# Optimization experiments

Hardware: AMD Instinct MI355X
Metric: run time of the kernel (lower is better)

Reference implementation:

```python
import jax, jax.numpy as jnp
import numpy as np

HEAD_DIM = 64

def setup_inputs() -> dict:
    key = jax.random.key(0)
    kq, kk, kv = jax.random.split(key, 3)
    shape = (2, 4096, 8, HEAD_DIM)  # [B, S, H, D]
    q = jax.random.normal(kq, shape, dtype=jnp.float32)
    k = jax.random.normal(kk, shape, dtype=jnp.float32)
    v = jax.random.normal(kv, shape, dtype=jnp.float32)
    return {"q": q, "k": k, "v": v}

def reference(q, k, v):
    # Single-process path of SimpleRingAttention: standard softmax attention.
    # q,k,v: [B, S, H, D]; scores computed per head.
    scale = 1.0 / jnp.sqrt(jnp.asarray(HEAD_DIM, dtype=q.dtype))
    scores = jnp.einsum('bqhd,bkhd->bhqk', q, k) * scale  # [B,H,S,S]
    attn = jax.nn.softmax(scores, axis=-1)
    out = jnp.einsum('bhqk,bkhd->bqhd', attn, v)  # back to [B,S,H,D]
    return out
```

## Files before the change

kernel.cpp:

```cpp
#include <hip/hip_runtime.h>
#include <hip/hip_bf16.h>

#define B_ 2
#define S_ 4096
#define H_ 8
#define D_ 64
#define BQ 128
#define BK 64

#define GLOBAL_AS __attribute__((address_space(1)))
#define LDS_AS    __attribute__((address_space(3)))

typedef short bf16x8 __attribute__((ext_vector_type(8)));
typedef short bf16x4 __attribute__((ext_vector_type(4)));
typedef float f32x4  __attribute__((ext_vector_type(4)));
typedef float f32x16 __attribute__((ext_vector_type(16)));
typedef unsigned int u32x4 __attribute__((ext_vector_type(4)));

#define QSCALE 0.18033688011112043f

__device__ __forceinline__ short f2bf(float f) {
    __bf16 h = (__bf16)f;
    return __builtin_bit_cast(short, h);
}

__device__ __forceinline__ bf16x8 pack8(float4 f0, float4 f1) {
    bf16x8 r;
    r[0]=f2bf(f0.x); r[1]=f2bf(f0.y); r[2]=f2bf(f0.z); r[3]=f2bf(f0.w);
    r[4]=f2bf(f1.x); r[5]=f2bf(f1.y); r[6]=f2bf(f1.z); r[7]=f2bf(f1.w);
    return r;
}

__device__ __forceinline__ bf16x8 pack8s(float4 f0, float4 f1, float s) {
    bf16x8 r;
    r[0]=f2bf(f0.x*s); r[1]=f2bf(f0.y*s); r[2]=f2bf(f0.z*s); r[3]=f2bf(f0.w*s);
    r[4]=f2bf(f1.x*s); r[5]=f2bf(f1.y*s); r[6]=f2bf(f1.z*s); r[7]=f2bf(f1.w*s);
    return r;
}

__device__ __forceinline__ unsigned pkbf(float a, float b) {
    unsigned ua = (unsigned)(unsigned short)__builtin_bit_cast(unsigned short, (__bf16)a);
    unsigned ub = (unsigned)(unsigned short)__builtin_bit_cast(unsigned short, (__bf16)b);
    return ua | (ub << 16);
}

__device__ __forceinline__ void perm32swap(unsigned &a, unsigned &b) {
    asm("v_permlane32_swap_b32 %0, %1" : "+v"(a), "+v"(b));
}

__global__ __launch_bounds__(256) void cast_kv_kernel(
    const float* __restrict__ kin, const float* __restrict__ vin,
    unsigned short* __restrict__ kb, unsigned short* __restrict__ vtb)
{
    __shared__ float Lf[64][72];
    const int role = blockIdx.z & 1;
    const int b    = blockIdx.z >> 1;
    const int h    = blockIdx.y;
    const int s0   = blockIdx.x * 64;
    const int t    = threadIdx.x;

    if (role == 0) {
        int r = t >> 2, fq = t & 3;
        const float4* gp = (const float4*)(kin + (((size_t)(b*S_ + s0 + r)*H_ + h)*D_ + fq*16));
        bf16x8 o0 = pack8(gp[0], gp[1]);
        bf16x8 o1 = pack8(gp[2], gp[3]);
        unsigned short* ob = kb + ((size_t)(b*H_ + h)*S_ + s0 + r)*D_ + fq*16;
        *(bf16x8*)ob       = o0;
        *(bf16x8*)(ob + 8) = o1;
    } else {
        {
            int r  = t >> 2, fq = t & 3;
            const float4* gp = (const float4*)(vin + (((size_t)(b*S_ + s0 + r)*H_ + h)*D_ + fq*16));
            #pragma unroll
            for (int j = 0; j < 4; ++j)
                *(f32x4*)&Lf[r][fq*16 + 4*j] = (f32x4){gp[j].x, gp[j].y, gp[j].z, gp[j].w};
        }
        __syncthreads();
        {
            int d = t >> 2, sq = t & 3;
            bf16x8 o0, o1;
            #pragma unroll
            for (int j = 0; j < 8; ++j) o0[j] = f2bf(Lf[sq*16 + j][d]);
            #pragma unroll
            for (int j = 0; j < 8; ++j) o1[j] = f2bf(Lf[sq*16 + 8 + j][d]);
            unsigned short* ob = vtb + (((size_t)(b*H_ + h)*D_ + d)*S_ + s0 + sq*16);
            *(bf16x8*)(ob)     = o0;
            *(bf16x8*)(ob + 8) = o1;
        }
    }
}

template<bool SPLIT>
__global__ __launch_bounds__(256, 4) void fattn_kernel(
    const float* __restrict__ q, const unsigned short* __restrict__ kb,
    const unsigned short* __restrict__ vtb, float* __restrict__ out,
    float* __restrict__ Op, float* __restrict__ lw)
{
    __shared__ unsigned short Ks [BK][64];
    __shared__ unsigned short Vts[D_][64];

    const int tid  = threadIdx.x;
    const int wave = tid >> 6;
    const int lane = tid & 63;
    const int l31  = tid & 31;
    const int hi   = lane >> 5;
    const int h    = blockIdx.y;
    const int b    = SPLIT ? (blockIdx.z >> 1) : blockIdx.z;
    const int half = SPLIT ? (blockIdx.z & 1)  : 0;
    const int kt0  = half * 32;
    const int nkt  = SPLIT ? 32 : 64;
    const int q0   = blockIdx.x * BQ;
    const int bS   = b * S_;
    const int wq   = wave * 32;

    int aoff[2][4];
    #pragma unroll
    for (int t = 0; t < 2; ++t)
        #pragma unroll
        for (int kc = 0; kc < 4; ++kc)
            aoff[t][kc] = (t*32 + l31)*64 + (((kc*2 + hi) ^ (l31 & 7))*8);

    const int srow = (lane >> 3);
    const int c8g  = (lane & 7) ^ srow;
    const int wqs  = wave * 16;
    const unsigned short* ksg[2];
    const unsigned short* vtg[2];
    #pragma unroll
    for (int it = 0; it < 2; ++it) {
        int rk = wqs + it*8 + srow;
        ksg[it] = kb  + ((size_t)(b*H_ + h)*S_ + rk)*64 + c8g*8;
        vtg[it] = vtb + ((size_t)(b*H_ + h)*D_ + rk)*(size_t)S_ + c8g*8;
    }

    bf16x8 bq[4];
    {
        const int qrow = q0 + wq + l31;
        const float* qp = q + ((size_t)(bS + qrow)*H_ + h)*D_;
        #pragma unroll
        for (int kc = 0; kc < 4; ++kc) {
            const float4* q4 = (const float4*)(qp + kc*16 + hi*8);
            bq[kc] = pack8s(q4[0], q4[1], QSCALE);
        }
    }

    f32x16 oacc[2];
    #pragma unroll
    for (int dt = 0; dt < 2; ++dt)
        #pragma unroll
        for (int r = 0; r < 16; ++r) oacc[dt][r] = 0.f;
    float lp0 = 0.f, lp1 = 0.f;

    for (int i = 0; i < nkt; ++i) {
        const int kt = kt0 + i;
        __syncthreads();
        #pragma unroll
        for (int it = 0; it < 2; ++it) {
            __builtin_amdgcn_global_load_lds(
                (const GLOBAL_AS void*)(ksg[it] + (size_t)kt*BK*64),
                (LDS_AS void*)&Ks[wqs + it*8][0], 16, 0, 0);
            __builtin_amdgcn_global_load_lds(
                (const GLOBAL_AS void*)(vtg[it] + (size_t)kt*BK),
                (LDS_AS void*)&Vts[wqs + it*8][0], 16, 0, 0);
        }
        __syncthreads();

        #pragma unroll
        for (int mt = 0; mt < 2; ++mt) {
            f32x16 s;
            #pragma unroll
            for (int r = 0; r < 16; ++r) s[r] = 0.f;
            #pragma unroll
            for (int kc = 0; kc < 4; ++kc) {
                bf16x8 aK = *(const bf16x8*)&Ks[0][aoff[mt][kc]];
                s = __builtin_amdgcn_mfma_f32_32x32x16_bf16(aK, bq[kc], s, 0,0,0);
            }

            unsigned pk_[8];
            #pragma unroll
            for (int r = 0; r < 8; ++r) {
                float e0 = __builtin_exp2f(s[2*r]);
                float e1 = __builtin_exp2f(s[2*r+1]);
                lp0 += e0; lp1 += e1;
                pk_[r] = pkbf(e0, e1);
            }
            perm32swap(pk_[0], pk_[2]);
            perm32swap(pk_[1], pk_[3]);
            perm32swap(pk_[4], pk_[6]);
            perm32swap(pk_[5], pk_[7]);
            u32x4 w0 = {pk_[0], pk_[1], pk_[2], pk_[3]};
            u32x4 w1 = {pk_[4], pk_[5], pk_[6], pk_[7]};
            bf16x8 bp0 = __builtin_bit_cast(bf16x8, w0);
            bf16x8 bp1 = __builtin_bit_cast(bf16x8, w1);

            #pragma unroll
            for (int dt = 0; dt < 2; ++dt) {
                bf16x8 aV0 = *(const bf16x8*)&Vts[0][aoff[dt][mt*2 + 0]];
                oacc[dt] = __builtin_amdgcn_mfma_f32_32x32x16_bf16(aV0, bp0, oacc[dt], 0,0,0);
                bf16x8 aV1 = *(const bf16x8*)&Vts[0][aoff[dt][mt*2 + 1]];
                oacc[dt] = __builtin_amdgcn_mfma_f32_32x32x16_bf16(aV1, bp1, oacc[dt], 0,0,0);
            }
        }
    }

    float lt0 = lp0 + lp1;
    float lt  = lt0 + __shfl_xor(lt0, 32);
    const int orow = q0 + wq + l31;
    if constexpr (SPLIT) {
        float* ob = Op + (size_t)half*((size_t)B_*S_*H_*D_)
                       + ((size_t)(bS + orow)*H_ + h)*D_;
        #pragma unroll
        for (int dt = 0; dt < 2; ++dt)
            #pragma unroll
            for (int rg = 0; rg < 4; ++rg) {
                float4 o4 = { oacc[dt][rg*4+0], oacc[dt][rg*4+1],
                              oacc[dt][rg*4+2], oacc[dt][rg*4+3] };
                *(float4*)(ob + dt*32 + rg*8 + hi*4) = o4;
            }
        if (hi == 0)
            lw[(size_t)half*((size_t)B_*S_*H_) + (size_t)(bS + orow)*H_ + h] = lt;
    } else {
        const float linv = 1.0f / lt;
        float* ob = out + ((size_t)(bS + orow)*H_ + h)*D_;
        #pragma unroll
        for (int dt = 0; dt < 2; ++dt)
            #pragma unroll
            for (int rg = 0; rg < 4; ++rg) {
                float4 o4 = { oacc[dt][rg*4+0]*linv, oacc[dt][rg*4+1]*linv,
                              oacc[dt][rg*4+2]*linv, oacc[dt][rg*4+3]*linv };
                *(float4*)(ob + dt*32 + rg*8 + hi*4) = o4;
            }
    }
}

__global__ __launch_bounds__(256) void combine_kernel(
    const float* __restrict__ Op, const float* __restrict__ lw,
    float* __restrict__ out)
{
    const size_t NR = (size_t)B_*S_*H_;
    const size_t NO = NR * D_;
    const int t = threadIdx.x;
    size_t r  = (size_t)blockIdx.x * 16 + (t >> 4);
    int   c4  = t & 15;
    const float4* p0 = (const float4*)(Op + r*D_) + c4;
    const float4* p1 = (const float4*)(Op + NO + r*D_) + c4;
    float linv = 1.0f / (lw[r] + lw[NR + r]);
    float4 a = *p0, b = *p1;
    float4 o = { (a.x+b.x)*linv, (a.y+b.y)*linv, (a.z+b.z)*linv, (a.w+b.w)*linv };
    *((float4*)(out + r*D_) + c4) = o;
}

#define FBQ 64
#define LDK 72
__global__ __launch_bounds__(256, 4) void fattn_fb(
    const float* __restrict__ q, const float* __restrict__ k,
    const float* __restrict__ v, float* __restrict__ out)
{
    __shared__ unsigned short Ks [BK][LDK];
    __shared__ unsigned short Vts[D_][LDK];
    __shared__ unsigned short Ps [FBQ][LDK];
    const int tid  = threadIdx.x;
    const int wave = tid >> 6;
    const int m16  = tid & 15;
    const int quad = (tid & 63) >> 4;
    const int h    = blockIdx.y;
    const int b    = blockIdx.z;
    const int q0   = blockIdx.x * FBQ;
    const int bS   = b * S_;
    const int wq   = wave * 16;
    bf16x8 bq[2];
    {
        const int qrow = q0 + wq + m16;
        const float* qb = q + ((size_t)(bS + qrow)*H_ + h)*D_;
        #pragma unroll
        for (int kh = 0; kh < 2; ++kh) {
            const float4* qp = (const float4*)(qb + kh*32 + quad*8);
            bq[kh] = pack8s(qp[0], qp[1], QSCALE);
        }
    }
    const short ONE = 0x3F80;
    bf16x8 ones = { ONE,ONE,ONE,ONE,ONE,ONE,ONE,ONE };
    f32x4 oacc[4];
    f32x4 lacc = (f32x4){0.f,0.f,0.f,0.f};
    #pragma unroll
    for (int dt = 0; dt < 4; ++dt) oacc[dt] = (f32x4){0.f,0.f,0.f,0.f};
    const int vd  = tid & 63;
    const int vkg = tid >> 6;
    for (int kt = 0; kt < S_/BK; ++kt) {
        const int k0 = kt * BK;
        __syncthreads();
        #pragma unroll
        for (int i = 0; i < 2; ++i) {
            int chunk = tid + i*256;
            int row = chunk >> 3, c8 = chunk & 7;
            const float4* gp = (const float4*)(k + ((size_t)(bS + k0 + row)*H_ + h)*D_ + c8*8);
            *(bf16x8*)&Ks[row][c8*8] = pack8(gp[0], gp[1]);
        }
        {
            const float* vb = v + ((size_t)(bS + k0 + vkg*16)*H_ + h)*D_ + vd;
            bf16x8 t0, t1;
            #pragma unroll
            for (int i = 0; i < 8; ++i) t0[i] = f2bf(vb[(size_t)i * (H_*D_)]);
            #pragma unroll
            for (int i = 0; i < 8; ++i) t1[i] = f2bf(vb[(size_t)(i+8) * (H_*D_)]);
            *(bf16x8*)&Vts[vd][vkg*16]     = t0;
            *(bf16x8*)&Vts[vd][vkg*16 + 8] = t1;
        }
        __syncthreads();
        f32x4 sacc[4];
        #pragma unroll
        for (int mt = 0; mt < 4; ++mt) sacc[mt] = (f32x4){0.f,0.f,0.f,0.f};
        #pragma unroll
        for (int kh = 0; kh < 2; ++kh)
            #pragma unroll
            for (int mt = 0; mt < 4; ++mt) {
                bf16x8 aK = *(const bf16x8*)&Ks[mt*16 + m16][kh*32 + quad*8];
                sacc[mt] = __builtin_amdgcn_mfma_f32_16x16x32_bf16(aK, bq[kh], sacc[mt], 0,0,0);
            }
        #pragma unroll
        for (int mt = 0; mt < 4; ++mt) {
            bf16x4 pk;
            #pragma unroll
            for (int r = 0; r < 4; ++r)
                pk[r] = f2bf(__builtin_exp2f(sacc[mt][r]));
            *(bf16x4*)&Ps[wq + m16][mt*16 + quad*4] = pk;
        }
        #pragma unroll
        for (int kh = 0; kh < 2; ++kh) {
            bf16x8 bp = *(const bf16x8*)&Ps[wq + m16][kh*32 + quad*8];
            lacc = __builtin_amdgcn_mfma_f32_16x16x32_bf16(ones, bp, lacc, 0,0,0);
            #pragma unroll
            for (int dt = 0; dt < 4; ++dt) {
                bf16x8 aV = *(const bf16x8*)&Vts[dt*16 + m16][kh*32 + quad*8];
                oacc[dt] = __builtin_amdgcn_mfma_f32_16x16x32_bf16(aV, bp, oacc[dt], 0,0,0);
            }
        }
    }
    const float linv = 1.0f / lacc[0];
    const int orow = q0 + wq + m16;
    float* ob = out + ((size_t)(bS + orow)*H_ + h)*D_;
    #pragma unroll
    for (int dt = 0; dt < 4; ++dt) {
        float4 o4 = { oacc[dt][0]*linv, oacc[dt][1]*linv,
                      oacc[dt][2]*linv, oacc[dt][3]*linv };
        *(float4*)(ob + dt*16 + quad*4) = o4;
    }
}

extern "C" void kernel_launch(void* const* d_in, const int* in_sizes, int n_in,
                              void* d_out, int out_size, void* d_ws, size_t ws_size,
                              hipStream_t stream) {
    const float* q = (const float*)d_in[0];
    const float* k = (const float*)d_in[1];
    const float* v = (const float*)d_in[2];
    float* out = (float*)d_out;
    const size_t elems = (size_t)B_*H_*S_*D_;
    const size_t NR    = (size_t)B_*S_*H_;
    const size_t need_cast  = 2 * elems * sizeof(unsigned short);
    const size_t need_split = need_cast + 2*elems*sizeof(float) + 2*NR*sizeof(float);

    if (ws_size >= need_split) {
        unsigned short* kb  = (unsigned short*)d_ws;
        unsigned short* vtb = kb + elems;
        float* Op = (float*)(vtb + elems);
        float* lw = Op + 2*elems;
        cast_kv_kernel<<<dim3(S_/64, H_, B_*2), dim3(256), 0, stream>>>(k, v, kb, vtb);
        fattn_kernel<true><<<dim3(S_/BQ, H_, B_*2), dim3(256), 0, stream>>>(
            q, kb, vtb, out, Op, lw);
        combine_kernel<<<dim3((int)(NR/16)), dim3(256), 0, stream>>>(Op, lw, out);
    } else if (ws_size >= need_cast) {
        unsigned short* kb  = (unsigned short*)d_ws;
        unsigned short* vtb = kb + elems;
        cast_kv_kernel<<<dim3(S_/64, H_, B_*2), dim3(256), 0, stream>>>(k, v, kb, vtb);
        fattn_kernel<false><<<dim3(S_/BQ, H_, B_), dim3(256), 0, stream>>>(
            q, kb, vtb, out, nullptr, nullptr);
    } else {
        fattn_fb<<<dim3(S_/FBQ, H_, B_), dim3(256), 0, stream>>>(q, k, v, out);
    }
}
```

Before: 209.3 us.

## Double-buffer K/V tiles in LDS with async prefetch of next tile

Adds a second LDS buffer for K and V tiles and issues the global-to-LDS loads for tile i+1 before computing tile i. Manual vmcnt waits and raw s_barrier replace the two __syncthreads per iteration, and s_setprio raises wave priority around the MFMA section. The goal is to hide global load latency behind the matrix work. In exchange it doubles LDS use per block, which may reduce occupancy, and it depends on the hand-written waitcnt counts being correct.

```diff
diff --git a/kernel.cpp b/kernel.cpp
--- a/kernel.cpp
+++ b/kernel.cpp
@@ -96,8 +96,8 @@
     const unsigned short* __restrict__ vtb, float* __restrict__ out,
     float* __restrict__ Op, float* __restrict__ lw)
 {
-    __shared__ unsigned short Ks [BK][64];
-    __shared__ unsigned short Vts[D_][64];
+    __shared__ unsigned short Ks [2][BK][64];
+    __shared__ unsigned short Vts[2][D_][64];
 
     const int tid  = threadIdx.x;
     const int wave = tid >> 6;
@@ -150,20 +150,38 @@
         for (int r = 0; r < 16; ++r) oacc[dt][r] = 0.f;
     float lp0 = 0.f, lp1 = 0.f;
 
+    #pragma unroll
+    for (int it = 0; it < 2; ++it) {
+        __builtin_amdgcn_global_load_lds(
+            (const GLOBAL_AS void*)(ksg[it] + (size_t)kt0*BK*64),
+            (LDS_AS void*)&Ks[0][wqs + it*8][0], 16, 0, 0);
+        __builtin_amdgcn_global_load_lds(
+            (const GLOBAL_AS void*)(vtg[it] + (size_t)kt0*BK),
+            (LDS_AS void*)&Vts[0][wqs + it*8][0], 16, 0, 0);
+    }
+
     for (int i = 0; i < nkt; ++i) {
-        const int kt = kt0 + i;
-        __syncthreads();
-        #pragma unroll
-        for (int it = 0; it < 2; ++it) {
-            __builtin_amdgcn_global_load_lds(
-                (const GLOBAL_AS void*)(ksg[it] + (size_t)kt*BK*64),
-                (LDS_AS void*)&Ks[wqs + it*8][0], 16, 0, 0);
-            __builtin_amdgcn_global_load_lds(
-                (const GLOBAL_AS void*)(vtg[it] + (size_t)kt*BK),
-                (LDS_AS void*)&Vts[wqs + it*8][0], 16, 0, 0);
-        }
-        __syncthreads();
-
+        const int cur = i & 1;
+        if (i + 1 < nkt) {
+            const int kt = kt0 + i + 1;
+            #pragma unroll
+            for (int it = 0; it < 2; ++it) {
+                __builtin_amdgcn_global_load_lds(
+                    (const GLOBAL_AS void*)(ksg[it] + (size_t)kt*BK*64),
+                    (LDS_AS void*)&Ks[cur ^ 1][wqs + it*8][0], 16, 0, 0);
+                __builtin_amdgcn_global_load_lds(
+                    (const GLOBAL_AS void*)(vtg[it] + (size_t)kt*BK),
+                    (LDS_AS void*)&Vts[cur ^ 1][wqs + it*8][0], 16, 0, 0);
+            }
+            asm volatile("s_waitcnt vmcnt(4)" ::: "memory");
+        } else {
+            asm volatile("s_waitcnt vmcnt(0)" ::: "memory");
+        }
+        __builtin_amdgcn_sched_barrier(0);
+        __builtin_amdgcn_s_barrier();
+        __builtin_amdgcn_sched_barrier(0);
+
+        __builtin_amdgcn_s_setprio(1);
         #pragma unroll
         for (int mt = 0; mt < 2; ++mt) {
             f32x16 s;
@@ -171,7 +189,7 @@
             for (int r = 0; r < 16; ++r) s[r] = 0.f;
             #pragma unroll
             for (int kc = 0; kc < 4; ++kc) {
-                bf16x8 aK = *(const bf16x8*)&Ks[0][aoff[mt][kc]];
+                bf16x8 aK = *(const bf16x8*)&Ks[cur][0][aoff[mt][kc]];
                 s = __builtin_amdgcn_mfma_f32_32x32x16_bf16(aK, bq[kc], s, 0,0,0);
             }
 
@@ -194,12 +212,15 @@
 
             #pragma unroll
             for (int dt = 0; dt < 2; ++dt) {
-                bf16x8 aV0 = *(const bf16x8*)&Vts[0][aoff[dt][mt*2 + 0]];
+                bf16x8 aV0 = *(const bf16x8*)&Vts[cur][0][aoff[dt][mt*2 + 0]];
                 oacc[dt] = __builtin_amdgcn_mfma_f32_32x32x16_bf16(aV0, bp0, oacc[dt], 0,0,0);
-                bf16x8 aV1 = *(const bf16x8*)&Vts[0][aoff[dt][mt*2 + 1]];
+                bf16x8 aV1 = *(const bf16x8*)&Vts[cur][0][aoff[dt][mt*2 + 1]];
                 oacc[dt] = __builtin_amdgcn_mfma_f32_32x32x16_bf16(aV1, bp1, oacc[dt], 0,0,0);
             }
         }
+        __builtin_amdgcn_s_setprio(0);
+        __builtin_amdgcn_sched_barrier(0);
+        __builtin_amdgcn_s_barrier();
     }
 
     float lt0 = lp0 + lp1;
```

Result: no change. 206.0 us (-1.6%).

## Split each key tile across two wave groups and reduce partial outputs in LDS

Applied to the files above, without the earlier changes.

Doubles the block to 512 threads (8 waves). Waves 0-3 and 4-7 each own the same 32-row query slices but take different 32-key halves of every 64-key tile. Partial O accumulators and row sums from the upper waves are then merged through LDS before the usual store. Each wave now does half the MFMA work per tile, so more waves are resident to hide latency, at the cost of an end-of-kernel LDS reduction, extra barriers, and a duplicate Q load per wave group.

```diff
diff --git a/kernel.cpp b/kernel.cpp
--- a/kernel.cpp
+++ b/kernel.cpp
@@ -91,19 +91,21 @@
 }
 
 template<bool SPLIT>
-__global__ __launch_bounds__(256, 4) void fattn_kernel(
+__global__ __launch_bounds__(512, 8) void fattn_kernel(
     const float* __restrict__ q, const unsigned short* __restrict__ kb,
     const unsigned short* __restrict__ vtb, float* __restrict__ out,
     float* __restrict__ Op, float* __restrict__ lw)
 {
-    __shared__ unsigned short Ks [BK][64];
-    __shared__ unsigned short Vts[D_][64];
+    __shared__ unsigned short KV[2][64][64];
+    __shared__ float lbuf[4][32];
 
     const int tid  = threadIdx.x;
     const int wave = tid >> 6;
     const int lane = tid & 63;
     const int l31  = tid & 31;
     const int hi   = lane >> 5;
+    const int qw   = wave & 3;
+    const int kw   = wave >> 2;
     const int h    = blockIdx.y;
     const int b    = SPLIT ? (blockIdx.z >> 1) : blockIdx.z;
     const int half = SPLIT ? (blockIdx.z & 1)  : 0;
@@ -111,26 +113,24 @@
     const int nkt  = SPLIT ? 32 : 64;
     const int q0   = blockIdx.x * BQ;
     const int bS   = b * S_;
-    const int wq   = wave * 32;
-
-    int aoff[2][4];
-    #pragma unroll
-    for (int t = 0; t < 2; ++t)
-        #pragma unroll
-        for (int kc = 0; kc < 4; ++kc)
-            aoff[t][kc] = (t*32 + l31)*64 + (((kc*2 + hi) ^ (l31 & 7))*8);
-
-    const int srow = (lane >> 3);
-    const int c8g  = (lane & 7) ^ srow;
-    const int wqs  = wave * 16;
-    const unsigned short* ksg[2];
-    const unsigned short* vtg[2];
-    #pragma unroll
-    for (int it = 0; it < 2; ++it) {
-        int rk = wqs + it*8 + srow;
-        ksg[it] = kb  + ((size_t)(b*H_ + h)*S_ + rk)*64 + c8g*8;
-        vtg[it] = vtb + ((size_t)(b*H_ + h)*D_ + rk)*(size_t)S_ + c8g*8;
-    }
+    const int wq   = qw * 32;
+
+    const int r7 = l31 & 7;
+    int koff[4];
+    #pragma unroll
+    for (int kc = 0; kc < 4; ++kc)
+        koff[kc] = (kw*32 + l31)*64 + (((kc*2 + hi) ^ r7)*8);
+    int voff[2][2];
+    #pragma unroll
+    for (int dt = 0; dt < 2; ++dt)
+        #pragma unroll
+        for (int c = 0; c < 2; ++c)
+            voff[dt][c] = (dt*32 + l31)*64 + ((((kw*2 + c)*2 + hi) ^ r7)*8);
+
+    const int srow = tid >> 3;
+    const int c8g  = (tid & 7) ^ (srow & 7);
+    const unsigned short* ksg = kb  + ((size_t)(b*H_ + h)*S_ + srow)*64 + c8g*8;
+    const unsigned short* vtg = vtb + ((size_t)(b*H_ + h)*D_ + srow)*(size_t)S_ + c8g*8;
 
     bf16x8 bq[4];
     {
@@ -150,85 +150,111 @@
         for (int r = 0; r < 16; ++r) oacc[dt][r] = 0.f;
     float lp0 = 0.f, lp1 = 0.f;
 
+    const unsigned short* Kb = &KV[0][0][0];
+    const unsigned short* Vb = &KV[1][0][0];
+
     for (int i = 0; i < nkt; ++i) {
         const int kt = kt0 + i;
         __syncthreads();
-        #pragma unroll
-        for (int it = 0; it < 2; ++it) {
-            __builtin_amdgcn_global_load_lds(
-                (const GLOBAL_AS void*)(ksg[it] + (size_t)kt*BK*64),
-                (LDS_AS void*)&Ks[wqs + it*8][0], 16, 0, 0);
-            __builtin_amdgcn_global_load_lds(
-                (const GLOBAL_AS void*)(vtg[it] + (size_t)kt*BK),
-                (LDS_AS void*)&Vts[wqs + it*8][0], 16, 0, 0);
-        }
-        __syncthreads();
-
-        #pragma unroll
-        for (int mt = 0; mt < 2; ++mt) {
-            f32x16 s;
-            #pragma unroll
-            for (int r = 0; r < 16; ++r) s[r] = 0.f;
-            #pragma unroll
-            for (int kc = 0; kc < 4; ++kc) {
-                bf16x8 aK = *(const bf16x8*)&Ks[0][aoff[mt][kc]];
-                s = __builtin_amdgcn_mfma_f32_32x32x16_bf16(aK, bq[kc], s, 0,0,0);
-            }
-
-            unsigned pk_[8];
-            #pragma unroll
-            for (int r = 0; r < 8; ++r) {
-                float e0 = __builtin_exp2f(s[2*r]);
-                float e1 = __builtin_exp2f(s[2*r+1]);
-                lp0 += e0; lp1 += e1;
-                pk_[r] = pkbf(e0, e1);
-            }
-            perm32swap(pk_[0], pk_[2]);
-            perm32swap(pk_[1], pk_[3]);
-            perm32swap(pk_[4], pk_[6]);
-            perm32swap(pk_[5], pk_[7]);
-            u32x4 w0 = {pk_[0], pk_[1], pk_[2], pk_[3]};
-            u32x4 w1 = {pk_[4], pk_[5], pk_[6], pk_[7]};
-            bf16x8 bp0 = __builtin_bit_cast(bf16x8, w0);
-            bf16x8 bp1 = __builtin_bit_cast(bf16x8, w1);
-
-            #pragma unroll
-            for (int dt = 0; dt < 2; ++dt) {
-                bf16x8 aV0 = *(const bf16x8*)&Vts[0][aoff[dt][mt*2 + 0]];
-                oacc[dt] = __builtin_amdgcn_mfma_f32_32x32x16_bf16(aV0, bp0, oacc[dt], 0,0,0);
-                bf16x8 aV1 = *(const bf16x8*)&Vts[0][aoff[dt][mt*2 + 1]];
-                oacc[dt] = __builtin_amdgcn_mfma_f32_32x32x16_bf16(aV1, bp1, oacc[dt], 0,0,0);
-            }
+        __builtin_amdgcn_global_load_lds(
+            (const GLOBAL_AS void*)(ksg + (size_t)kt*BK*64),
+            (LDS_AS void*)&KV[0][wave*8][0], 16, 0, 0);
+        __builtin_amdgcn_global_load_lds(
+            (const GLOBAL_AS void*)(vtg + (size_t)kt*BK),
+            (LDS_AS void*)&KV[1][wave*8][0], 16, 0, 0);
+        __syncthreads();
+
+        f32x16 s;
+        #pragma unroll
+        for (int r = 0; r < 16; ++r) s[r] = 0.f;
+        #pragma unroll
+        for (int kc = 0; kc < 4; ++kc) {
+            bf16x8 aK = *(const bf16x8*)&Kb[koff[kc]];
+            s = __builtin_amdgcn_mfma_f32_32x32x16_bf16(aK, bq[kc], s, 0,0,0);
+        }
+
+        unsigned pk_[8];
+        #pragma unroll
+        for (int r = 0; r < 8; ++r) {
+            float e0 = __builtin_exp2f(s[2*r]);
+            float e1 = __builtin_exp2f(s[2*r+1]);
+            lp0 += e0; lp1 += e1;
+            pk_[r] = pkbf(e0, e1);
+        }
+        perm32swap(pk_[0], pk_[2]);
+        perm32swap(pk_[1], pk_[3]);
+        perm32swap(pk_[4], pk_[6]);
+        perm32swap(pk_[5], pk_[7]);
+        u32x4 w0 = {pk_[0], pk_[1], pk_[2], pk_[3]};
+        u32x4 w1 = {pk_[4], pk_[5], pk_[6], pk_[7]};
+        bf16x8 bp0 = __builtin_bit_cast(bf16x8, w0);
+        bf16x8 bp1 = __builtin_bit_cast(bf16x8, w1);
+
+        #pragma unroll
+        for (int dt = 0; dt < 2; ++dt) {
+            bf16x8 aV0 = *(const bf16x8*)&Vb[voff[dt][0]];
+            oacc[dt] = __builtin_amdgcn_mfma_f32_32x32x16_bf16(aV0, bp0, oacc[dt], 0,0,0);
+            bf16x8 aV1 = *(const bf16x8*)&Vb[voff[dt][1]];
+            oacc[dt] = __builtin_amdgcn_mfma_f32_32x32x16_bf16(aV1, bp1, oacc[dt], 0,0,0);
         }
     }
 
     float lt0 = lp0 + lp1;
     float lt  = lt0 + __shfl_xor(lt0, 32);
-    const int orow = q0 + wq + l31;
-    if constexpr (SPLIT) {
-        float* ob = Op + (size_t)half*((size_t)B_*S_*H_*D_)
-                       + ((size_t)(bS + orow)*H_ + h)*D_;
-        #pragma unroll
-        for (int dt = 0; dt < 2; ++dt)
+
+    float* cb = (float*)&KV[0][0][0];
+    #pragma unroll
+    for (int dt = 0; dt < 2; ++dt) {
+        __syncthreads();
+        if (wave >= 4) {
+            float* base = cb + (wave - 4)*1024 + (hi*32 + l31)*16;
+            #pragma unroll
+            for (int rg = 0; rg < 4; ++rg)
+                *(f32x4*)(base + rg*4) =
+                    (f32x4){ oacc[dt][rg*4+0], oacc[dt][rg*4+1],
+                             oacc[dt][rg*4+2], oacc[dt][rg*4+3] };
+            if (dt == 0 && hi == 0) lbuf[wave - 4][l31] = lt;
+        }
+        __syncthreads();
+        if (wave < 4) {
+            const float* base = cb + qw*1024 + (hi*32 + l31)*16;
             #pragma unroll
             for (int rg = 0; rg < 4; ++rg) {
-                float4 o4 = { oacc[dt][rg*4+0], oacc[dt][rg*4+1],
-                              oacc[dt][rg*4+2], oacc[dt][rg*4+3] };
-                *(float4*)(ob + dt*32 + rg*8 + hi*4) = o4;
+                f32x4 p = *(const f32x4*)(base + rg*4);
+                oacc[dt][rg*4+0] += p[0]; oacc[dt][rg*4+1] += p[1];
+                oacc[dt][rg*4+2] += p[2]; oacc[dt][rg*4+3] += p[3];
             }
-        if (hi == 0)
-            lw[(size_t)half*((size_t)B_*S_*H_) + (size_t)(bS + orow)*H_ + h] = lt;
-    } else {
-        const float linv = 1.0f / lt;
-        float* ob = out + ((size_t)(bS + orow)*H_ + h)*D_;
-        #pragma unroll
-        for (int dt = 0; dt < 2; ++dt)
-            #pragma unroll
-            for (int rg = 0; rg < 4; ++rg) {
-                float4 o4 = { oacc[dt][rg*4+0]*linv, oacc[dt][rg*4+1]*linv,
-                              oacc[dt][rg*4+2]*linv, oacc[dt][rg*4+3]*linv };
-                *(float4*)(ob + dt*32 + rg*8 + hi*4) = o4;
-            }
+        }
+    }
+
+    if (wave < 4) {
+        lt += lbuf[qw][l31];
+        const int orow = q0 + wq + l31;
+        if constexpr (SPLIT) {
+            float* ob = Op + (size_t)half*((size_t)B_*S_*H_*D_)
+                           + ((size_t)(bS + orow)*H_ + h)*D_;
+            #pragma unroll
+            for (int dt = 0; dt < 2; ++dt)
+                #pragma unroll
+                for (int rg = 0; rg < 4; ++rg) {
+                    float4 o4 = { oacc[dt][rg*4+0], oacc[dt][rg*4+1],
+                                  oacc[dt][rg*4+2], oacc[dt][rg*4+3] };
+                    *(float4*)(ob + dt*32 + rg*8 + hi*4) = o4;
+                }
+            if (hi == 0)
+                lw[(size_t)half*((size_t)B_*S_*H_) + (size_t)(bS + orow)*H_ + h] = lt;
+        } else {
+            const float linv = 1.0f / lt;
+            float* ob = out + ((size_t)(bS + orow)*H_ + h)*D_;
+            #pragma unroll
+            for (int dt = 0; dt < 2; ++dt)
+                #pragma unroll
+                for (int rg = 0; rg < 4; ++rg) {
+                    float4 o4 = { oacc[dt][rg*4+0]*linv, oacc[dt][rg*4+1]*linv,
+                                  oacc[dt][rg*4+2]*linv, oacc[dt][rg*4+3]*linv };
+                    *(float4*)(ob + dt*32 + rg*8 + hi*4) = o4;
+                }
+        }
     }
 }
 
@@ -364,14 +390,14 @@
         float* Op = (float*)(vtb + elems);
         float* lw = Op + 2*elems;
         cast_kv_kernel<<<dim3(S_/64, H_, B_*2), dim3(256), 0, stream>>>(k, v, kb, vtb);
-        fattn_kernel<true><<<dim3(S_/BQ, H_, B_*2), dim3(256), 0, stream>>>(
+        fattn_kernel<true><<<dim3(S_/BQ, H_, B_*2), dim3(512), 0, stream>>>(
             q, kb, vtb, out, Op, lw);
         combine_kernel<<<dim3((int)(NR/16)), dim3(256), 0, stream>>>(Op, lw, out);
     } else if (ws_size >= need_cast) {
         unsigned short* kb  = (unsigned short*)d_ws;
         unsigned short* vtb = kb + elems;
         cast_kv_kernel<<<dim3(S_/64, H_, B_*2), dim3(256), 0, stream>>>(k, v, kb, vtb);
-        fattn_kernel<false><<<dim3(S_/BQ, H_, B_), dim3(256), 0, stream>>>(
+        fattn_kernel<false><<<dim3(S_/BQ, H_, B_), dim3(512), 0, stream>>>(
             q, kb, vtb, out, nullptr, nullptr);
     } else {
         fattn_fb<<<dim3(S_/FBQ, H_, B_), dim3(256), 0, stream>>>(q, k, v, out);
```

Measured after the change: 362.0 us. 73.0% more time.

## Double key tile to 128 with new swizzled LDS layout for K and V

Applied to the files above, without the earlier changes.

Raises the per-iteration key block from 64 to 128 in the main flash-attention kernel, halving the number of loop iterations and the barrier pairs around each LDS fill. The LDS address swizzles for K and transposed V are recomputed for the wider V row, and the global-to-LDS load mapping is redone. The fallback kernel keeps its own 64-wide tile through a new constant. LDS use per block doubles, which may limit occupancy, and there is still no overlap between loads and compute.

```diff
diff --git a/kernel.cpp b/kernel.cpp
--- a/kernel.cpp
+++ b/kernel.cpp
@@ -6,7 +6,7 @@
 #define H_ 8
 #define D_ 64
 #define BQ 128
-#define BK 64
+#define BK 128
 
 #define GLOBAL_AS __attribute__((address_space(1)))
 #define LDS_AS    __attribute__((address_space(3)))
@@ -97,7 +97,7 @@
     float* __restrict__ Op, float* __restrict__ lw)
 {
     __shared__ unsigned short Ks [BK][64];
-    __shared__ unsigned short Vts[D_][64];
+    __shared__ unsigned short Vts[D_][BK];
 
     const int tid  = threadIdx.x;
     const int wave = tid >> 6;
@@ -107,30 +107,35 @@
     const int h    = blockIdx.y;
     const int b    = SPLIT ? (blockIdx.z >> 1) : blockIdx.z;
     const int half = SPLIT ? (blockIdx.z & 1)  : 0;
-    const int kt0  = half * 32;
-    const int nkt  = SPLIT ? 32 : 64;
+    const int kt0  = half * 16;
+    const int nkt  = SPLIT ? 16 : 32;
     const int q0   = blockIdx.x * BQ;
     const int bS   = b * S_;
     const int wq   = wave * 32;
 
-    int aoff[2][4];
-    #pragma unroll
-    for (int t = 0; t < 2; ++t)
-        #pragma unroll
-        for (int kc = 0; kc < 4; ++kc)
-            aoff[t][kc] = (t*32 + l31)*64 + (((kc*2 + hi) ^ (l31 & 7))*8);
-
-    const int srow = (lane >> 3);
-    const int c8g  = (lane & 7) ^ srow;
-    const int wqs  = wave * 16;
-    const unsigned short* ksg[2];
-    const unsigned short* vtg[2];
-    #pragma unroll
-    for (int it = 0; it < 2; ++it) {
-        int rk = wqs + it*8 + srow;
-        ksg[it] = kb  + ((size_t)(b*H_ + h)*S_ + rk)*64 + c8g*8;
-        vtg[it] = vtb + ((size_t)(b*H_ + h)*D_ + rk)*(size_t)S_ + c8g*8;
-    }
+    const int r7 = l31 & 7;
+    const int q2 = r7 >> 1;
+    const int r2 = r7 >> 2;
+    const int h0 = hi ^ (r7 & 1);
+
+    int k0[4];
+    #pragma unroll
+    for (int kc = 0; kc < 4; ++kc)
+        k0[kc] = l31*64 + ((kc ^ q2)*2 + h0)*8;
+    int v0[2][2];
+    #pragma unroll
+    for (int c = 0; c < 2; ++c)
+        #pragma unroll
+        for (int m1 = 0; m1 < 2; ++m1)
+            v0[c][m1] = l31*128 + (((c*2 + hi) ^ (r7 & 3))*8) + ((m1 ^ r2)*32);
+
+    const unsigned short* ksg =
+        kb + ((size_t)(b*H_ + h)*S_ + wave*8 + (lane>>3))*64 + ((lane&7) ^ (lane>>3))*8;
+    const int vce = (lane & 15) ^ (lane >> 4);
+    const unsigned short* vt0 =
+        vtb + ((size_t)(b*H_ + h)*D_ + wave*16 + 0 + (lane>>4))*(size_t)S_ + vce*8;
+    const unsigned short* vt1 =
+        vtb + ((size_t)(b*H_ + h)*D_ + wave*16 + 4 + (lane>>4))*(size_t)S_ + (vce ^ 4)*8;
 
     bf16x8 bq[4];
     {
@@ -150,28 +155,40 @@
         for (int r = 0; r < 16; ++r) oacc[dt][r] = 0.f;
     float lp0 = 0.f, lp1 = 0.f;
 
+    const unsigned short* Kf = &Ks[0][0];
+    const unsigned short* Vf = &Vts[0][0];
+
     for (int i = 0; i < nkt; ++i) {
         const int kt = kt0 + i;
         __syncthreads();
-        #pragma unroll
-        for (int it = 0; it < 2; ++it) {
+        {
+            const unsigned short* kp = ksg + (size_t)kt*BK*64;
+            #pragma unroll
+            for (int it = 0; it < 4; ++it)
+                __builtin_amdgcn_global_load_lds(
+                    (const GLOBAL_AS void*)(kp + it*32*64),
+                    (LDS_AS void*)&Ks[it*32 + wave*8][0], 16, 0, 0);
+            const unsigned short* vp0 = vt0 + (size_t)kt*BK;
+            const unsigned short* vp1 = vt1 + (size_t)kt*BK;
             __builtin_amdgcn_global_load_lds(
-                (const GLOBAL_AS void*)(ksg[it] + (size_t)kt*BK*64),
-                (LDS_AS void*)&Ks[wqs + it*8][0], 16, 0, 0);
+                (const GLOBAL_AS void*)(vp0),            (LDS_AS void*)&Vts[wave*16 +  0][0], 16, 0, 0);
             __builtin_amdgcn_global_load_lds(
-                (const GLOBAL_AS void*)(vtg[it] + (size_t)kt*BK),
-                (LDS_AS void*)&Vts[wqs + it*8][0], 16, 0, 0);
-        }
-        __syncthreads();
-
-        #pragma unroll
-        for (int mt = 0; mt < 2; ++mt) {
+                (const GLOBAL_AS void*)(vp1),            (LDS_AS void*)&Vts[wave*16 +  4][0], 16, 0, 0);
+            __builtin_amdgcn_global_load_lds(
+                (const GLOBAL_AS void*)(vp0 + 8*(size_t)S_), (LDS_AS void*)&Vts[wave*16 +  8][0], 16, 0, 0);
+            __builtin_amdgcn_global_load_lds(
+                (const GLOBAL_AS void*)(vp1 + 8*(size_t)S_), (LDS_AS void*)&Vts[wave*16 + 12][0], 16, 0, 0);
+        }
+        __syncthreads();
+
+        #pragma unroll
+        for (int mt = 0; mt < 4; ++mt) {
             f32x16 s;
             #pragma unroll
             for (int r = 0; r < 16; ++r) s[r] = 0.f;
             #pragma unroll
             for (int kc = 0; kc < 4; ++kc) {
-                bf16x8 aK = *(const bf16x8*)&Ks[0][aoff[mt][kc]];
+                bf16x8 aK = *(const bf16x8*)&Kf[k0[kc] + mt*2048];
                 s = __builtin_amdgcn_mfma_f32_32x32x16_bf16(aK, bq[kc], s, 0,0,0);
             }
 
@@ -194,9 +211,9 @@
 
             #pragma unroll
             for (int dt = 0; dt < 2; ++dt) {
-                bf16x8 aV0 = *(const bf16x8*)&Vts[0][aoff[dt][mt*2 + 0]];
+                bf16x8 aV0 = *(const bf16x8*)&Vf[v0[0][mt & 1] + (mt >> 1)*64 + dt*4096];
                 oacc[dt] = __builtin_amdgcn_mfma_f32_32x32x16_bf16(aV0, bp0, oacc[dt], 0,0,0);
-                bf16x8 aV1 = *(const bf16x8*)&Vts[0][aoff[dt][mt*2 + 1]];
+                bf16x8 aV1 = *(const bf16x8*)&Vf[v0[1][mt & 1] + (mt >> 1)*64 + dt*4096];
                 oacc[dt] = __builtin_amdgcn_mfma_f32_32x32x16_bf16(aV1, bp1, oacc[dt], 0,0,0);
             }
         }
@@ -250,12 +267,13 @@
 }
 
 #define FBQ 64
+#define FBK 64
 #define LDK 72
 __global__ __launch_bounds__(256, 4) void fattn_fb(
     const float* __restrict__ q, const float* __restrict__ k,
     const float* __restrict__ v, float* __restrict__ out)
 {
-    __shared__ unsigned short Ks [BK][LDK];
+    __shared__ unsigned short Ks [FBK][LDK];
     __shared__ unsigned short Vts[D_][LDK];
     __shared__ unsigned short Ps [FBQ][LDK];
     const int tid  = threadIdx.x;
@@ -285,8 +303,8 @@
     for (int dt = 0; dt < 4; ++dt) oacc[dt] = (f32x4){0.f,0.f,0.f,0.f};
     const int vd  = tid & 63;
     const int vkg = tid >> 6;
-    for (int kt = 0; kt < S_/BK; ++kt) {
-        const int k0 = kt * BK;
+    for (int kt = 0; kt < S_/FBK; ++kt) {
+        const int k0 = kt * FBK;
         __syncthreads();
         #pragma unroll
         for (int i = 0; i < 2; ++i) {
```

Result: no change. 206.0 us (-1.5%).
